# Kernel tuning notes

Measured on AMD Instinct MI355X. Metric: run time of the kernel, lower is better.

## Reference

```python
import jax, jax.numpy as jnp
import numpy as np
import math

N_HEAD = 8
N_FEAT = 512
D_K = N_FEAT // N_HEAD
B, T = 4, 2048


def setup_inputs() -> dict:
    key = jax.random.key(0)
    ks = jax.random.split(key, 16)
    s = 1.0 / math.sqrt(N_FEAT)
    return {
        "x": jax.random.normal(ks[0], (B, T, N_FEAT), dtype=jnp.float32),
        "pos_emb": jax.random.normal(ks[1], (1, T, N_FEAT), dtype=jnp.float32),
        "Wq": jax.random.normal(ks[2], (N_FEAT, N_FEAT), dtype=jnp.float32) * s,
        "bq": jnp.zeros((N_FEAT,), dtype=jnp.float32),
        "Wk": jax.random.normal(ks[3], (N_FEAT, N_FEAT), dtype=jnp.float32) * s,
        "bk": jnp.zeros((N_FEAT,), dtype=jnp.float32),
        "Wv": jax.random.normal(ks[4], (N_FEAT, N_FEAT), dtype=jnp.float32) * s,
        "bv": jnp.zeros((N_FEAT,), dtype=jnp.float32),
        "Wpos": jax.random.normal(ks[5], (N_FEAT, N_FEAT), dtype=jnp.float32) * s,
        "Wout": jax.random.normal(ks[6], (N_FEAT, N_FEAT), dtype=jnp.float32) * s,
        "bout": jnp.zeros((N_FEAT,), dtype=jnp.float32),
        "pos_bias_u": jax.random.normal(ks[7], (N_HEAD, D_K), dtype=jnp.float32) * 0.05,
        "pos_bias_v": jax.random.normal(ks[8], (N_HEAD, D_K), dtype=jnp.float32) * 0.05,
    }


def reference(x, pos_emb, Wq, bq, Wk, bk, Wv, bv, Wpos, Wout, bout,
              pos_bias_u, pos_bias_v):
    b, t, f = x.shape
    h, d = N_HEAD, D_K
    # QKV projections (torch Linear: y = x @ W.T + b), split into heads -> (B,H,T,d)
    q = (jnp.einsum('btf,of->bto', x, Wq) + bq).reshape(b, t, h, d).transpose(0, 2, 1, 3)
    k = (jnp.einsum('btf,of->bto', x, Wk) + bk).reshape(b, t, h, d).transpose(0, 2, 1, 3)
    v = (jnp.einsum('btf,of->bto', x, Wv) + bv).reshape(b, t, h, d).transpose(0, 2, 1, 3)
    # positional projection: (1, T_pos, F) -> (H, T_pos, d)
    tp = pos_emb.shape[1]
    p = jnp.einsum('ptf,of->pto', pos_emb, Wpos).reshape(tp, h, d).transpose(1, 0, 2)
    q_u = q + pos_bias_u[None, :, None, :]  # (B,H,T,d)
    q_v = q + pos_bias_v[None, :, None, :]
    matrix_ac = jnp.einsum('bhtd,bhsd->bhts', q_u, k)   # content-content
    matrix_bd = jnp.einsum('bhtd,hsd->bhts', q_v, p)    # content-position
    scores = (matrix_ac + matrix_bd) / math.sqrt(d)
    attn = jax.nn.softmax(scores, axis=-1)  # dropout is identity in eval mode
    out = jnp.einsum('bhts,bhsd->bhtd', attn, v)
    out = out.transpose(0, 2, 1, 3).reshape(b, t, h * d)
    return jnp.einsum('btf,of->bto', out, Wout) + bout
```

## Files before the change

### kernel.cpp

```cpp
#include <hip/hip_runtime.h>

typedef float f4 __attribute__((ext_vector_type(4)));
typedef __attribute__((ext_vector_type(8))) short bf16x8;
typedef __attribute__((ext_vector_type(4))) float f32x4;

#define T_SEQ 2048
#define NFEAT 512
#define NHEAD 8
#define DK    64
#define BATCH 4

using gptr_t = const __attribute__((address_space(1))) void*;
using lptr_t = __attribute__((address_space(3))) void*;

#define LOG2E_8 0.18033688011f

static __device__ __forceinline__ short f2bf(float f) {
    unsigned u = __builtin_bit_cast(unsigned, f);
    u += 0x7fff + ((u >> 16) & 1);
    return (short)(u >> 16);
}
static __device__ __forceinline__ short f2bfr(float f) {
    unsigned u = __builtin_bit_cast(unsigned, f);
    return (short)((u + 0x8000u) >> 16);
}
static __device__ __forceinline__ float b2f(short s) {
    unsigned u = ((unsigned)(unsigned short)s) << 16;
    return __builtin_bit_cast(float, u);
}

__global__ __launch_bounds__(256) void cvt_kernel(
    const float* __restrict__ x, const float* __restrict__ pos,
    const float* __restrict__ Wq, const float* __restrict__ Wk, const float* __restrict__ Wv,
    const float* __restrict__ Wpos, const float* __restrict__ Wout,
    const float* __restrict__ bq, const float* __restrict__ bk, const float* __restrict__ bv,
    short* __restrict__ xb, short* __restrict__ posb, short* __restrict__ wqkv,
    short* __restrict__ wpb, short* __restrict__ wob, float* __restrict__ bqkv)
{
    const int blk = blockIdx.x;
    const float* src; short* dst; int off;
    if      (blk < 2048) { src = x;    dst = xb;          off = blk * 2048; }
    else if (blk < 2560) { src = pos;  dst = posb;        off = (blk - 2048) * 2048; }
    else if (blk < 2688) { src = Wq;   dst = wqkv;        off = (blk - 2560) * 2048; }
    else if (blk < 2816) { src = Wk;   dst = wqkv + 262144; off = (blk - 2688) * 2048; }
    else if (blk < 2944) { src = Wv;   dst = wqkv + 524288; off = (blk - 2816) * 2048; }
    else if (blk < 3072) { src = Wpos; dst = wpb;         off = (blk - 2944) * 2048; }
    else if (blk < 3200) { src = Wout; dst = wob;         off = (blk - 3072) * 2048; }
    else {
        int t = threadIdx.x;
        bqkv[t]        = bq[t];        bqkv[256 + t]  = bq[256 + t];
        bqkv[512 + t]  = bk[t];        bqkv[768 + t]  = bk[256 + t];
        bqkv[1024 + t] = bv[t];        bqkv[1280 + t] = bv[256 + t];
        return;
    }
    int i = off + threadIdx.x * 8;
    f4 a = *(const f4*)(src + i);
    f4 b = *(const f4*)(src + i + 4);
    bf16x8 o;
#pragma unroll
    for (int j = 0; j < 4; ++j) { o[j] = f2bf(a[j]); o[4 + j] = f2bf(b[j]); }
    *(bf16x8*)(dst + i) = o;
}

template<int OUT_BF16>
static __device__ __forceinline__ void gemm_tile(
    short* As, short* Bs,
    const short* __restrict__ A, const short* __restrict__ B,
    const float* __restrict__ bias, void* __restrict__ Cv,
    int N, int K, int row0, int col0)
{
    const int tid = threadIdx.x, lane = tid & 63, wave = tid >> 6;
    const int col = lane & 15, quad = lane >> 4;
    const int wm = (wave >> 1) * 64, wn = (wave & 1) * 64;
    const int rl = lane & 15;

    const short* Abase = A + (size_t)(row0 + wave * 32 + rl) * K + (lane >> 4) * 8;
    const short* Bbase = B + (size_t)(col0 + wave * 32 + rl) * K + (lane >> 4) * 8;

    f32x4 acc[4][4];
#pragma unroll
    for (int i = 0; i < 4; ++i)
#pragma unroll
        for (int j = 0; j < 4; ++j) acc[i][j] = (f32x4){0.f, 0.f, 0.f, 0.f};

    for (int k0 = 0; k0 < K; k0 += 64) {
        __syncthreads();
#pragma unroll
        for (int c = 0; c < 2; ++c)
#pragma unroll
            for (int hf = 0; hf < 2; ++hf) {
                __builtin_amdgcn_global_load_lds((gptr_t)(Abase + (size_t)(16 * c) * K + k0 + hf * 32),
                                                 (lptr_t)(As + wave * 2048 + c * 1024 + hf * 512), 16, 0, 0);
                __builtin_amdgcn_global_load_lds((gptr_t)(Bbase + (size_t)(16 * c) * K + k0 + hf * 32),
                                                 (lptr_t)(Bs + wave * 2048 + c * 1024 + hf * 512), 16, 0, 0);
            }
        __syncthreads();
#pragma unroll
        for (int kt = 0; kt < 2; ++kt) {
            bf16x8 af[4], bfr[4];
#pragma unroll
            for (int mt = 0; mt < 4; ++mt)
                af[mt] = *(const bf16x8*)&As[((wm >> 4) + mt) * 1024 + (kt * 4 + quad) * 128 + col * 8];
#pragma unroll
            for (int nt = 0; nt < 4; ++nt)
                bfr[nt] = *(const bf16x8*)&Bs[((wn >> 4) + nt) * 1024 + (kt * 4 + quad) * 128 + col * 8];
#pragma unroll
            for (int mt = 0; mt < 4; ++mt)
#pragma unroll
                for (int nt = 0; nt < 4; ++nt)
                    acc[mt][nt] = __builtin_amdgcn_mfma_f32_16x16x32_bf16(af[mt], bfr[nt], acc[mt][nt], 0, 0, 0);
        }
    }

    float bv4[4];
#pragma unroll
    for (int nt = 0; nt < 4; ++nt)
        bv4[nt] = bias ? bias[col0 + wn + nt * 16 + col] : 0.f;
#pragma unroll
    for (int mt = 0; mt < 4; ++mt)
#pragma unroll
        for (int reg = 0; reg < 4; ++reg) {
            int r = row0 + wm + mt * 16 + quad * 4 + reg;
#pragma unroll
            for (int nt = 0; nt < 4; ++nt) {
                int c = col0 + wn + nt * 16 + col;
                float v = acc[mt][nt][reg] + bv4[nt];
                if (OUT_BF16) ((short*)Cv)[(size_t)r * N + c] = f2bf(v);
                else          ((float*)Cv)[(size_t)r * N + c] = v;
            }
        }
}

__global__ __launch_bounds__(256) void gemm_qkv_pos(
    const short* __restrict__ xb, const short* __restrict__ wqkv,
    const float* __restrict__ bqkv, short* __restrict__ QKV,
    const short* __restrict__ posb, const short* __restrict__ wpb,
    short* __restrict__ Pm)
{
    __shared__ short As[8192], Bs[8192];
    const int bid = blockIdx.x;
    if (bid < 768) {
        const int xcd = bid & 7, s = bid >> 3;
        const int row = xcd * 8 + (s & 7), colt = s >> 3;
        gemm_tile<1>(As, Bs, xb, wqkv, bqkv, QKV, 1536, 512, row * 128, colt * 128);
    } else {
        const int t = bid - 768;
        gemm_tile<1>(As, Bs, posb, wpb, nullptr, Pm, 512, 512, (t / 4) * 128, (t % 4) * 128);
    }
}

__global__ __launch_bounds__(256) void gemm_out_kernel(
    const short* __restrict__ A, const short* __restrict__ B,
    const float* __restrict__ bias, float* __restrict__ C)
{
    __shared__ short As[8192], Bs[8192];
    const int bid = blockIdx.x;
    const int xcd = bid & 7, s = bid >> 3;
    const int row = xcd * 8 + (s & 7), colt = s >> 3;
    gemm_tile<0>(As, Bs, A, B, bias, C, 512, 512, row * 128, colt * 128);
}

__global__ __launch_bounds__(256) void kvprep_kernel(
    const short* __restrict__ qkv, const short* __restrict__ pm,
    const float* __restrict__ u, const float* __restrict__ vb,
    short* __restrict__ kp, short* __restrict__ vt, float* __restrict__ cb)
{
    __shared__ short tile[64][72];
    const int tid = threadIdx.x, lr = tid >> 2, lc = (tid & 3) * 16;
    const int bh = blockIdx.y, b = bh >> 3, h = bh & 7, s0 = blockIdx.x * 64;

    const short* kptr = qkv + (size_t)(b * T_SEQ + s0 + lr) * 1536 + 512 + h * DK + lc;
    const short* pptr = pm + (size_t)(s0 + lr) * NFEAT + h * DK + lc;
    const short* vptr = qkv + (size_t)(b * T_SEQ + s0 + lr) * 1536 + 1024 + h * DK + lc;
    bf16x8 k0_ = *(const bf16x8*)kptr,       k1_ = *(const bf16x8*)(kptr + 8);
    bf16x8 p0_ = *(const bf16x8*)pptr,       p1_ = *(const bf16x8*)(pptr + 8);
    bf16x8 v0_ = *(const bf16x8*)vptr,       v1_ = *(const bf16x8*)(vptr + 8);

    float c = 0.f;
    bf16x8 o0, o1;
#pragma unroll
    for (int j = 0; j < 8; ++j) {
        float kf = b2f(k0_[j]), pf = b2f(p0_[j]);
        o0[j] = f2bf(kf + pf);
        c += u[h * DK + lc + j] * kf + vb[h * DK + lc + j] * pf;
        float kf1 = b2f(k1_[j]), pf1 = b2f(p1_[j]);
        o1[j] = f2bf(kf1 + pf1);
        c += u[h * DK + lc + 8 + j] * kf1 + vb[h * DK + lc + 8 + j] * pf1;
    }
    short* kpd = kp + ((size_t)bh * T_SEQ + s0 + lr) * DK + lc;
    *(bf16x8*)kpd       = o0;
    *(bf16x8*)(kpd + 8) = o1;
    c += __shfl_xor(c, 1);
    c += __shfl_xor(c, 2);
    if ((tid & 3) == 0) cb[(size_t)bh * T_SEQ + s0 + lr] = LOG2E_8 * c;

    *(bf16x8*)&tile[lr][lc]     = v0_;
    *(bf16x8*)&tile[lr][lc + 8] = v1_;
    __syncthreads();
    short* dst = vt + (size_t)(bh * DK + lr) * T_SEQ + s0 + lc;
    bf16x8 t0_, t1_;
#pragma unroll
    for (int j = 0; j < 8; ++j) { t0_[j] = tile[lc + j][lr]; t1_[j] = tile[lc + 8 + j][lr]; }
    *(bf16x8*)dst       = t0_;
    *(bf16x8*)(dst + 8) = t1_;
}

__global__ __launch_bounds__(512) void attn_kernel(
    const short* __restrict__ qkv, const short* __restrict__ kp,
    const short* __restrict__ vt, const float* __restrict__ cb,
    short* __restrict__ attO)
{
    __shared__ __align__(16) short Qs[128][72], KPs[64][72], Vts[64][72], Ps[8][16][72];
    __shared__ float cs[64];
    const int tid = threadIdx.x, lane = tid & 63, wave = tid >> 6;
    const int col = lane & 15, quad = lane >> 4;
    const int idx = blockIdx.x;
    const int xcd = idx & 7, slot = idx >> 3;
    const int bh = (slot >> 4) * 8 + xcd;
    const int t0 = (slot & 15) * 128;
    const int b = bh >> 3, h = bh & 7;

    {
        const int lr = tid >> 2, lc = (tid & 3) * 16;
        const short* qp = qkv + (size_t)(b * T_SEQ + t0 + lr) * 1536 + h * DK + lc;
        *(bf16x8*)&Qs[lr][lc]     = *(const bf16x8*)qp;
        *(bf16x8*)&Qs[lr][lc + 8] = *(const bf16x8*)(qp + 8);
    }
    const int lr8 = tid >> 3, lc8 = (tid & 7) * 8;

    bf16x8 kpr = *(const bf16x8*)(kp + ((size_t)bh * T_SEQ + lr8) * DK + lc8);
    bf16x8 vtr = *(const bf16x8*)(vt + ((size_t)(bh * DK + lr8)) * T_SEQ + lc8);
    float cbr = (tid < 64) ? cb[(size_t)bh * T_SEQ + tid] : 0.f;

    __syncthreads();
    bf16x8 qa0 = *(const bf16x8*)&Qs[wave * 16 + col][quad * 8];
    bf16x8 qa1 = *(const bf16x8*)&Qs[wave * 16 + col][32 + quad * 8];

    f32x4 Oacc[4];
    float lsum[4] = {0.f, 0.f, 0.f, 0.f};
#pragma unroll
    for (int i = 0; i < 4; ++i) Oacc[i] = (f32x4){0.f, 0.f, 0.f, 0.f};

    for (int s0 = 0; s0 < T_SEQ; s0 += 64) {
        __syncthreads();
        *(bf16x8*)&KPs[lr8][lc8] = kpr;
        *(bf16x8*)&Vts[lr8][lc8] = vtr;
        if (tid < 64) cs[tid] = cbr;
        __syncthreads();

        const int sn = (s0 + 64) & (T_SEQ - 1);
        kpr = *(const bf16x8*)(kp + ((size_t)bh * T_SEQ + sn + lr8) * DK + lc8);
        vtr = *(const bf16x8*)(vt + ((size_t)(bh * DK + lr8)) * T_SEQ + sn + lc8);
        if (tid < 64) cbr = cb[(size_t)bh * T_SEQ + sn + tid];

        f32x4 S[4];
#pragma unroll
        for (int nt = 0; nt < 4; ++nt) S[nt] = (f32x4){0.f, 0.f, 0.f, 0.f};
#pragma unroll
        for (int nt = 0; nt < 4; ++nt) {
            bf16x8 b0 = *(const bf16x8*)&KPs[nt * 16 + col][quad * 8];
            S[nt] = __builtin_amdgcn_mfma_f32_16x16x32_bf16(qa0, b0, S[nt], 0, 0, 0);
            bf16x8 b1 = *(const bf16x8*)&KPs[nt * 16 + col][32 + quad * 8];
            S[nt] = __builtin_amdgcn_mfma_f32_16x16x32_bf16(qa1, b1, S[nt], 0, 0, 0);
        }
        const float c0 = cs[col], c1 = cs[16 + col], c2 = cs[32 + col], c3 = cs[48 + col];
#pragma unroll
        for (int reg = 0; reg < 4; ++reg) {
            int r = quad * 4 + reg;
            float e0 = __builtin_amdgcn_exp2f(fmaf(S[0][reg], LOG2E_8, c0));
            float e1 = __builtin_amdgcn_exp2f(fmaf(S[1][reg], LOG2E_8, c1));
            float e2 = __builtin_amdgcn_exp2f(fmaf(S[2][reg], LOG2E_8, c2));
            float e3 = __builtin_amdgcn_exp2f(fmaf(S[3][reg], LOG2E_8, c3));
            lsum[reg] += (e0 + e1) + (e2 + e3);
            Ps[wave][r][col]      = f2bfr(e0);
            Ps[wave][r][16 + col] = f2bfr(e1);
            Ps[wave][r][32 + col] = f2bfr(e2);
            Ps[wave][r][48 + col] = f2bfr(e3);
        }
#pragma unroll
        for (int kt = 0; kt < 2; ++kt) {
            bf16x8 pa = *(const bf16x8*)&Ps[wave][col][kt * 32 + quad * 8];
#pragma unroll
            for (int dt = 0; dt < 4; ++dt) {
                bf16x8 vb = *(const bf16x8*)&Vts[dt * 16 + col][kt * 32 + quad * 8];
                Oacc[dt] = __builtin_amdgcn_mfma_f32_16x16x32_bf16(pa, vb, Oacc[dt], 0, 0, 0);
            }
        }
    }
#pragma unroll
    for (int reg = 0; reg < 4; ++reg) {
        float l = lsum[reg];
#pragma unroll
        for (int off = 1; off < 16; off <<= 1) l += __shfl_xor(l, off);
        float inv = 1.f / l;
        int t = t0 + wave * 16 + quad * 4 + reg;
        short* op = attO + (size_t)(b * T_SEQ + t) * NFEAT + h * DK;
#pragma unroll
        for (int dt = 0; dt < 4; ++dt)
            op[dt * 16 + col] = f2bf(Oacc[dt][reg] * inv);
    }
}

extern "C" void kernel_launch(void* const* d_in, const int* in_sizes, int n_in,
                              void* d_out, int out_size, void* d_ws, size_t ws_size,
                              hipStream_t stream)
{
    const float* x    = (const float*)d_in[0];
    const float* pos  = (const float*)d_in[1];
    const float* Wq   = (const float*)d_in[2];
    const float* bq   = (const float*)d_in[3];
    const float* Wk   = (const float*)d_in[4];
    const float* bk   = (const float*)d_in[5];
    const float* Wv   = (const float*)d_in[6];
    const float* bv   = (const float*)d_in[7];
    const float* Wpos = (const float*)d_in[8];
    const float* Wout = (const float*)d_in[9];
    const float* bout = (const float*)d_in[10];
    const float* pbu  = (const float*)d_in[11];
    const float* pbv  = (const float*)d_in[12];
    float* out = (float*)d_out;

    short* xb   = (short*)d_ws;
    short* posb = xb   + 4194304;
    short* wqkv = posb + 1048576;
    short* wpb  = wqkv + 786432;
    short* wob  = wpb  + 262144;
    short* QKV  = wob  + 262144;
    short* Pm   = QKV  + 12582912;
    short* KP   = Pm   + 1048576;
    short* Vt   = KP   + 4194304;
    short* AttO = Vt   + 4194304;
    float* bqkv = (float*)(AttO + 4194304);
    float* Cb   = bqkv + 1536;

    cvt_kernel<<<dim3(3201), dim3(256), 0, stream>>>(x, pos, Wq, Wk, Wv, Wpos, Wout, bq, bk, bv,
                                                     xb, posb, wqkv, wpb, wob, bqkv);
    gemm_qkv_pos<<<dim3(832), dim3(256), 0, stream>>>(xb, wqkv, bqkv, QKV, posb, wpb, Pm);
    kvprep_kernel<<<dim3(T_SEQ / 64, BATCH * NHEAD), dim3(256), 0, stream>>>(QKV, Pm, pbu, pbv, KP, Vt, Cb);
    attn_kernel<<<dim3(512), dim3(512), 0, stream>>>(QKV, KP, Vt, Cb, AttO);
    gemm_out_kernel<<<dim3(256), dim3(256), 0, stream>>>(AttO, wob, bout, out);
}
```

Measured before the change: 215.3 us.

## Permute key rows so softmax probabilities store packed, load Q into registers

K/P rows are loaded into shared memory in a permuted order (key 4*col+nt), so each lane's four score columns are adjacent keys. The exponentiated probabilities can then be packed into two bf16 pairs and written with one 8-byte LDS store, and the bias is read as one float4, replacing four scalar short stores and four scalar loads per row. Q fragments are now loaded straight from global memory into registers, which removes the Q shared-memory tile and one barrier. The launch bound also requests higher occupancy, which caps registers and risks spills.

```diff
diff --git a/kernel.cpp b/kernel.cpp
--- a/kernel.cpp
+++ b/kernel.cpp
@@ -3,6 +3,7 @@
 typedef float f4 __attribute__((ext_vector_type(4)));
 typedef __attribute__((ext_vector_type(8))) short bf16x8;
 typedef __attribute__((ext_vector_type(4))) float f32x4;
+typedef __attribute__((ext_vector_type(2))) int i32x2;
 
 #define T_SEQ 2048
 #define NFEAT 512
@@ -20,13 +21,14 @@
     u += 0x7fff + ((u >> 16) & 1);
     return (short)(u >> 16);
 }
-static __device__ __forceinline__ short f2bfr(float f) {
-    unsigned u = __builtin_bit_cast(unsigned, f);
-    return (short)((u + 0x8000u) >> 16);
-}
 static __device__ __forceinline__ float b2f(short s) {
     unsigned u = ((unsigned)(unsigned short)s) << 16;
     return __builtin_bit_cast(float, u);
+}
+static __device__ __forceinline__ int pkbf(float a, float b) {
+    unsigned ua = __builtin_bit_cast(unsigned, a) + 0x8000u;
+    unsigned ub = __builtin_bit_cast(unsigned, b) + 0x8000u;
+    return (int)((ua >> 16) | (ub & 0xFFFF0000u));
 }
 
 __global__ __launch_bounds__(256) void cvt_kernel(
@@ -205,12 +207,12 @@
     *(bf16x8*)(dst + 8) = t1_;
 }
 
-__global__ __launch_bounds__(512) void attn_kernel(
+__global__ __launch_bounds__(512, 8) void attn_kernel(
     const short* __restrict__ qkv, const short* __restrict__ kp,
     const short* __restrict__ vt, const float* __restrict__ cb,
     short* __restrict__ attO)
 {
-    __shared__ __align__(16) short Qs[128][72], KPs[64][72], Vts[64][72], Ps[8][16][72];
+    __shared__ __align__(16) short KPs[64][72], Vts[64][72], Ps[8][16][72];
     __shared__ float cs[64];
     const int tid = threadIdx.x, lane = tid & 63, wave = tid >> 6;
     const int col = lane & 15, quad = lane >> 4;
@@ -220,21 +222,16 @@
     const int t0 = (slot & 15) * 128;
     const int b = bh >> 3, h = bh & 7;
 
-    {
-        const int lr = tid >> 2, lc = (tid & 3) * 16;
-        const short* qp = qkv + (size_t)(b * T_SEQ + t0 + lr) * 1536 + h * DK + lc;
-        *(bf16x8*)&Qs[lr][lc]     = *(const bf16x8*)qp;
-        *(bf16x8*)&Qs[lr][lc + 8] = *(const bf16x8*)(qp + 8);
-    }
+    const short* qbase = qkv + (size_t)(b * T_SEQ + t0 + wave * 16 + col) * 1536 + h * DK + quad * 8;
+    bf16x8 qa0 = *(const bf16x8*)qbase;
+    bf16x8 qa1 = *(const bf16x8*)(qbase + 32);
+
     const int lr8 = tid >> 3, lc8 = (tid & 7) * 8;
-
-    bf16x8 kpr = *(const bf16x8*)(kp + ((size_t)bh * T_SEQ + lr8) * DK + lc8);
+    const int rho = 4 * (lr8 & 15) + (lr8 >> 4);
+
+    bf16x8 kpr = *(const bf16x8*)(kp + ((size_t)bh * T_SEQ + rho) * DK + lc8);
     bf16x8 vtr = *(const bf16x8*)(vt + ((size_t)(bh * DK + lr8)) * T_SEQ + lc8);
     float cbr = (tid < 64) ? cb[(size_t)bh * T_SEQ + tid] : 0.f;
-
-    __syncthreads();
-    bf16x8 qa0 = *(const bf16x8*)&Qs[wave * 16 + col][quad * 8];
-    bf16x8 qa1 = *(const bf16x8*)&Qs[wave * 16 + col][32 + quad * 8];
 
     f32x4 Oacc[4];
     float lsum[4] = {0.f, 0.f, 0.f, 0.f};
@@ -249,7 +246,7 @@
         __syncthreads();
 
         const int sn = (s0 + 64) & (T_SEQ - 1);
-        kpr = *(const bf16x8*)(kp + ((size_t)bh * T_SEQ + sn + lr8) * DK + lc8);
+        kpr = *(const bf16x8*)(kp + ((size_t)bh * T_SEQ + sn + rho) * DK + lc8);
         vtr = *(const bf16x8*)(vt + ((size_t)(bh * DK + lr8)) * T_SEQ + sn + lc8);
         if (tid < 64) cbr = cb[(size_t)bh * T_SEQ + sn + tid];
 
@@ -263,19 +260,16 @@
             bf16x8 b1 = *(const bf16x8*)&KPs[nt * 16 + col][32 + quad * 8];
             S[nt] = __builtin_amdgcn_mfma_f32_16x16x32_bf16(qa1, b1, S[nt], 0, 0, 0);
         }
-        const float c0 = cs[col], c1 = cs[16 + col], c2 = cs[32 + col], c3 = cs[48 + col];
+        const f4 cv = *(const f4*)&cs[4 * col];
 #pragma unroll
         for (int reg = 0; reg < 4; ++reg) {
-            int r = quad * 4 + reg;
-            float e0 = __builtin_amdgcn_exp2f(fmaf(S[0][reg], LOG2E_8, c0));
-            float e1 = __builtin_amdgcn_exp2f(fmaf(S[1][reg], LOG2E_8, c1));
-            float e2 = __builtin_amdgcn_exp2f(fmaf(S[2][reg], LOG2E_8, c2));
-            float e3 = __builtin_amdgcn_exp2f(fmaf(S[3][reg], LOG2E_8, c3));
+            float e0 = __builtin_amdgcn_exp2f(fmaf(S[0][reg], LOG2E_8, cv[0]));
+            float e1 = __builtin_amdgcn_exp2f(fmaf(S[1][reg], LOG2E_8, cv[1]));
+            float e2 = __builtin_amdgcn_exp2f(fmaf(S[2][reg], LOG2E_8, cv[2]));
+            float e3 = __builtin_amdgcn_exp2f(fmaf(S[3][reg], LOG2E_8, cv[3]));
             lsum[reg] += (e0 + e1) + (e2 + e3);
-            Ps[wave][r][col]      = f2bfr(e0);
-            Ps[wave][r][16 + col] = f2bfr(e1);
-            Ps[wave][r][32 + col] = f2bfr(e2);
-            Ps[wave][r][48 + col] = f2bfr(e3);
+            i32x2 pw; pw[0] = pkbf(e0, e1); pw[1] = pkbf(e2, e3);
+            *(i32x2*)&Ps[wave][quad * 4 + reg][4 * col] = pw;
         }
 #pragma unroll
         for (int kt = 0; kt < 2; ++kt) {
```

Measured after the change: 243.0 us. +12.8%, slower.
